# Kernel tuning notes

Hardware: AMD Instinct MI355X
Metric: run time of the kernel (lower is better)

Reference implementation:

```python
import jax, jax.numpy as jnp
import numpy as np

MODES1 = 12
MODES2 = 12
WIDTH = 32
DATA_CH = 3
BN_EPS = 1e-5


def mirror(x):
    # x: (B, C, s, s) -> (B, C, 2s-1, 2s-1), odd-symmetric mirror
    top = jnp.concatenate([x[:, :, -1:0:-1, -1:0:-1], -x[:, :, -1:0:-1, :]], axis=3)
    bot = jnp.concatenate([-x[:, :, :, -1:0:-1], x], axis=3)
    return jnp.concatenate([top, bot], axis=2)


def spectral_conv(x, w1, w2):
    # x: (B, C, H, W); w1, w2: (C, C, m1, m2, 2) real/imag pairs
    H, W = x.shape[-2], x.shape[-1]
    xf = jnp.fft.rfft2(x, norm='ortho')  # (B, C, H, W//2+1) complex
    w1c = w1[..., 0] + 1j * w1[..., 1]
    w2c = w2[..., 0] + 1j * w2[..., 1]
    out = jnp.zeros(xf.shape[:2] + (H, W // 2 + 1), dtype=xf.dtype)
    out = out.at[:, :, :MODES1, :MODES2].set(
        jnp.einsum('bixy,ioxy->boxy', xf[:, :, :MODES1, :MODES2], w1c))
    out = out.at[:, :, H - MODES1:, :MODES2].set(
        jnp.einsum('bixy,ioxy->boxy', xf[:, :, H - MODES1:, :MODES2], w2c))
    return jnp.fft.irfft2(out, s=(H, W), norm='ortho')


def batch_norm(x, g, b):
    # training-mode BN over (B, H, W) per channel, biased variance
    mean = jnp.mean(x, axis=(0, 2, 3), keepdims=True)
    var = jnp.mean((x - mean) ** 2, axis=(0, 2, 3), keepdims=True)
    inv = jax.lax.rsqrt(var + BN_EPS)
    return g[None, :, None, None] * (x - mean) * inv + b[None, :, None, None]


def setup_inputs() -> dict:
    key = jax.random.key(0)
    ks = jax.random.split(key, 16)
    B, s = 16, 128
    scale = 1.0 / (WIDTH * WIDTH)
    inp = {
        'x': jax.random.normal(ks[0], (B, DATA_CH, s, s), dtype=jnp.float32),
        'fc0_w': jax.random.normal(ks[1], (DATA_CH, WIDTH), dtype=jnp.float32) * 0.3,
        'fc0_b': jax.random.normal(ks[2], (WIDTH,), dtype=jnp.float32) * 0.01,
        'spec_w': scale * jax.random.uniform(ks[3], (4, 2, WIDTH, WIDTH, MODES1, MODES2, 2), dtype=jnp.float32),
        'conv_w': jax.random.normal(ks[4], (4, WIDTH, WIDTH), dtype=jnp.float32) * (1.0 / np.sqrt(WIDTH)),
        'conv_b': jax.random.normal(ks[5], (4, WIDTH), dtype=jnp.float32) * 0.01,
        'bn_g': jnp.ones((4, WIDTH), dtype=jnp.float32),
        'bn_b': jnp.zeros((4, WIDTH), dtype=jnp.float32),
        'fc1_w': jax.random.normal(ks[6], (WIDTH, 128), dtype=jnp.float32) * (1.0 / np.sqrt(WIDTH)),
        'fc1_b': jax.random.normal(ks[7], (128,), dtype=jnp.float32) * 0.01,
        'fc2_w': jax.random.normal(ks[8], (128, 1), dtype=jnp.float32) * (1.0 / np.sqrt(128.0)),
        'fc2_b': jax.random.normal(ks[9], (1,), dtype=jnp.float32) * 0.01,
    }
    return inp


def reference(x, fc0_w, fc0_b, spec_w, conv_w, conv_b, bn_g, bn_b, fc1_w, fc1_b, fc2_w, fc2_b):
    x_small = x
    s = x.shape[-1]
    xm = mirror(x)  # (B, C, 2s-1, 2s-1)
    # fc0 lift (channels-last linear)
    h = jnp.einsum('bchw,cd->bdhw', xm, fc0_w) + fc0_b[None, :, None, None]
    for i in range(4):
        x1 = spectral_conv(h, spec_w[i, 0], spec_w[i, 1])
        x2 = jnp.einsum('bchw,oc->bohw', h, conv_w[i]) + conv_b[i][None, :, None, None]
        h = batch_norm(x1 + x2, bn_g[i], bn_b[i])
        if i < 3:
            h = jax.nn.relu(h)
    h = jnp.einsum('bchw,cd->bdhw', h, fc1_w) + fc1_b[None, :, None, None]
    h = jax.nn.relu(h)
    h = jnp.einsum('bchw,cd->bdhw', h, fc2_w) + fc2_b[None, :, None, None]  # (B,1,H,W)
    # unmirror: take bottom-right quadrant; torch assignment broadcasts 1 channel -> data_channels
    out = jnp.broadcast_to(h[:, :, s - 1:, s - 1:], x_small.shape)
    return out
```

## Files before the change

kernel.cpp:

```cpp
#include <hip/hip_runtime.h>

#define BATCH 16
#define CH 32
#define DC 3
#define SS 128
#define HH 255
#define RST 256
#define FST ((size_t)CH*RST)
#define M1 12
#define M2 12
#define KY24 (2*M1)
#define NROWS (BATCH*CH*HH)
#define TWOPI_N 0.02463994238463573f

typedef __attribute__((ext_vector_type(8))) _Float16 f16x8;
typedef __attribute__((ext_vector_type(4))) float f32x4;


__global__ void __launch_bounds__(256) k_fc0(
    const float* __restrict__ x, const float* __restrict__ w,
    const float* __restrict__ bias, _Float16* __restrict__ h){
  int y = blockIdx.x, b = blockIdx.y, t = threadIdx.x;
  int d = t >> 3, g = t & 7;
  int iy = (y >= SS-1) ? y - (SS-1) : (SS-1) - y;
  float w0 = w[d], w1 = w[CH+d], w2 = w[2*CH+d], bs = bias[d];
  const float* xp = x + (size_t)(b*DC)*SS*SS + iy*SS;
  size_t obase = (size_t)(b*HH + y)*FST + (size_t)d*RST;
  #pragma unroll
  for (int i=0; i<4; i++){
    int x0 = i*64 + g*8;
    f16x8 pk;
    #pragma unroll
    for (int u=0; u<8; u++){
      int xx = x0 + u;
      float v = 0.f;
      if (xx < HH){
        int ix = (xx >= SS-1) ? xx - (SS-1) : (SS-1) - xx;
        float sgn = ((y >= SS-1) == (xx >= SS-1)) ? 1.f : -1.f;
        v = bs + sgn*(xp[ix]*w0 + xp[SS*SS+ix]*w1 + xp[2*SS*SS+ix]*w2);
      }
      pk[u] = (_Float16)v;
    }
    *(f16x8*)(h + obase + x0) = pk;
  }
}

__global__ void __launch_bounds__(256) k_tabs(
    const float* __restrict__ w1,
    _Float16* __restrict__ Whi, _Float16* __restrict__ Wlo,
    _Float16* __restrict__ Th,  _Float16* __restrict__ Tl,
    _Float16* __restrict__ W1h, _Float16* __restrict__ W1l){
  int bi = blockIdx.x;
  if (bi < 4){
    int t = bi*256 + threadIdx.x;
    int ct = t >> 9, ks = (t >> 6) & 7, lane = t & 63;
    int col = ct*16 + (lane & 15);
    int kb = ks*32 + (lane >> 4)*8;
    for (int j=0; j<8; j++){
      int k = kb + j;
      float w = 0.f;
      if (k < 255 && col < 24){
        int m = col >> 1;
        float ang = TWOPI_N * (float)((k*m) % 255);
        w = (col & 1) ? -sinf(ang) : cosf(ang);
      }
      _Float16 hi = (_Float16)w;
      Whi[t*8+j] = hi;
      Wlo[t*8+j] = (_Float16)(w - (float)hi);
    }
  } else if (bi < 8){
    int t = (bi-4)*256 + threadIdx.x;
    int ct = t >> 6, lane = t & 63;
    int xx = ct*16 + (lane & 15);
    int jbase = (lane >> 4)*8;
    for (int j=0; j<8; j++){
      int jg = jbase + j;
      float v = 0.f;
      if (xx < HH && jg <= 22){
        if (jg == 0) v = 1.f;
        else if (jg & 1){ int kx=(jg+1)>>1; v =  cosf(TWOPI_N*(float)((kx*xx)%255)); }
        else            { int kx= jg>>1;    v = -sinf(TWOPI_N*(float)((kx*xx)%255)); }
      }
      _Float16 hi = (_Float16)v;
      Th[t*8+j] = hi;
      Tl[t*8+j] = (_Float16)(v - (float)hi);
    }
  } else {
    int t = (bi-8)*256 + threadIdx.x;
    int nt = t >> 6, lane = t & 63;
    int col = nt*16 + (lane & 15);
    int kb = (lane >> 4)*8;
    for (int j=0; j<8; j++){
      float v = w1[(kb+j)*128 + col];
      _Float16 hi = (_Float16)v;
      W1h[t*8+j] = hi;
      W1l[t*8+j] = (_Float16)(v - (float)hi);
    }
  }
}

__global__ void __launch_bounds__(256) k_fwd(
    const _Float16* __restrict__ h, float* __restrict__ Xf,
    const _Float16* __restrict__ Whi, const _Float16* __restrict__ Wlo,
    const float* __restrict__ parts, const float* __restrict__ g,
    const float* __restrict__ bb, float* __restrict__ bnpo,
    int l0, int relu){
  __shared__ float lr[HH][26];
  __shared__ float rs[256][2];
  int t = threadIdx.x, bc = blockIdx.x;
  int wid = t >> 6, lane = t & 63;
  int c = bc & (CH-1), b = bc >> 5;
  float sc = 1.f, sh = 0.f;
  if (!l0){
    float s1 = 0.f, s2 = 0.f;
    for (int k=t; k<BATCH*HH; k+=256){
      float2 p2 = *(const float2*)(parts + (size_t)k*64 + c*2);
      s1 += p2.x; s2 += p2.y;
    }
    rs[t][0] = s1; rs[t][1] = s2;
    __syncthreads();
    for (int w2=128; w2>0; w2>>=1){
      if (t < w2){ rs[t][0] += rs[t+w2][0]; rs[t][1] += rs[t+w2][1]; }
      __syncthreads();
    }
    const float N = (float)BATCH * (float)(HH*HH);
    float mean = rs[0][0] / N;
    float var  = rs[0][1] / N - mean*mean;
    float iv = rsqrtf(var + 1e-5f);
    sc = g[c]*iv;
    sh = bb[c] - mean*sc;
    __syncthreads();
  }
  if (b == 0 && t == 0){ bnpo[c] = sc; bnpo[CH+c] = sh; }
  _Float16 sch = (_Float16)sc, shh = (_Float16)sh;
  f16x8 scv, shv;
  #pragma unroll
  for (int u=0; u<8; u++){ scv[u]=sch; shv[u]=shh; }
  const _Float16* base = h + (size_t)b*HH*FST + (size_t)c*RST;
  int koff = (lane >> 4)*8;
  #pragma unroll
  for (int it=0; it<4; it++){
    int y0 = it*64 + wid*16;
    int yr = y0 + (lane & 15);
    int ycl = (yr < HH) ? yr : HH-1;
    const _Float16* rp = base + (size_t)ycl*FST;
    f16x8 av[8];
    #pragma unroll
    for (int ks=0; ks<8; ks++)
      av[ks] = *(const f16x8*)(rp + ks*32 + koff);
    f32x4 acc0 = {0.f,0.f,0.f,0.f};
    f32x4 acc1 = {0.f,0.f,0.f,0.f};
    #pragma unroll
    for (int ks=0; ks<8; ks++){
      f16x8 a = av[ks]*scv + shv;
      if (relu){
        #pragma unroll
        for (int u=0; u<8; u++) a[u] = (a[u] > (_Float16)0.f) ? a[u] : (_Float16)0.f;
      }
      f16x8 b0h = *(const f16x8*)(Whi + ((size_t)(0*8+ks)*64 + lane)*8);
      f16x8 b0l = *(const f16x8*)(Wlo + ((size_t)(0*8+ks)*64 + lane)*8);
      f16x8 b1h = *(const f16x8*)(Whi + ((size_t)(1*8+ks)*64 + lane)*8);
      f16x8 b1l = *(const f16x8*)(Wlo + ((size_t)(1*8+ks)*64 + lane)*8);
      acc0 = __builtin_amdgcn_mfma_f32_16x16x32_f16(a, b0h, acc0, 0,0,0);
      acc0 = __builtin_amdgcn_mfma_f32_16x16x32_f16(a, b0l, acc0, 0,0,0);
      acc1 = __builtin_amdgcn_mfma_f32_16x16x32_f16(a, b1h, acc1, 0,0,0);
      acc1 = __builtin_amdgcn_mfma_f32_16x16x32_f16(a, b1l, acc1, 0,0,0);
    }
    int colq = lane & 15;
    int rq = y0 + (lane >> 4)*4;
    #pragma unroll
    for (int q=0; q<4; q++)
      if (rq+q < HH) lr[rq+q][colq] = acc0[q];
    if (colq < 8){
      #pragma unroll
      for (int q=0; q<4; q++)
        if (rq+q < HH) lr[rq+q][16+colq] = acc1[q];
    }
  }
  __syncthreads();
  for (int p = t; p < KY24*M2; p += 256){
    int ky = p / M2, kx = p - (p/M2)*M2;
    int freq = (ky < M1) ? ky : (HH - KY24 + ky);
    float ang = TWOPI_N * (float)freq;
    float c1 = cosf(ang), s1 = sinf(ang);
    float cr=1.f, sr=0.f, ar=0.f, ai=0.f;
    for (int y=0; y<HH; y++){
      float rr = lr[y][kx*2], ri = lr[y][kx*2+1];
      ar += rr*cr + ri*sr;
      ai += ri*cr - rr*sr;
      float cn = cr*c1 - sr*s1;
      sr = sr*c1 + cr*s1;
      cr = cn;
    }
    const float inv = 1.0f/255.0f;
    int o = (bc*KY24 + ky)*(M2*2) + kx*2;
    Xf[o]   = ar*inv;
    Xf[o+1] = ai*inv;
  }
}

__global__ void __launch_bounds__(256) k_specmix(
    const float* __restrict__ Xf, const float* __restrict__ w,
    float* __restrict__ G){
  __shared__ float ly[KY24][M2][2];
  int o = blockIdx.x, b = blockIdx.y, t = threadIdx.x;
  for (int m = t; m < KY24*M2; m += 256){
    int ky = m / M2, kx = m - (m/M2)*M2;
    int blk = (ky < M1) ? 0 : 1;
    int m1 = ky - blk*M1;
    const float* wp = w + (size_t)blk*(CH*CH*M1*M2*2)
                        + (size_t)o*(M1*M2*2) + m1*(M2*2) + kx*2;
    const float* xp = Xf + ((size_t)(b*CH)*KY24 + ky)*(M2*2) + kx*2;
    float ar=0.f, ai=0.f;
    for (int i=0;i<CH;i++){
      float xr = xp[0], xi = xp[1];
      float wr = wp[0], wi = wp[1];
      ar += xr*wr - xi*wi;
      ai += xr*wi + xi*wr;
      xp += KY24*M2*2;
      wp += CH*M1*M2*2;
    }
    ly[ky][kx][0] = ar;
    ly[ky][kx][1] = ai;
  }
  __syncthreads();
  const float inv = 1.0f/255.0f;
  size_t bo = (size_t)b*CH + o;
  for (int p=t; p<HH*M2; p+=256){
    int y = p/M2, kx = p - (p/M2)*M2;
    float ang = TWOPI_N * (float)y;
    float c1 = cosf(ang), s1 = sinf(ang);
    float ar = ly[0][kx][0], ai = ly[0][kx][1];
    float c = c1, s = s1;
    #pragma unroll
    for (int k=1; k<=11; k++){
      float yr = ly[k][kx][0],     yi = ly[k][kx][1];
      ar += yr*c - yi*s;
      ai += yr*s + yi*c;
      float zr = ly[24-k][kx][0],  zi = ly[24-k][kx][1];
      ar += zr*c + zi*s;
      ai += zi*c - zr*s;
      float cn = c*c1 - s*s1;
      s = s*c1 + c*s1;
      c = cn;
    }
    {
      float zr = ly[12][kx][0], zi = ly[12][kx][1];
      ar += zr*c + zi*s;
      ai += zi*c - zr*s;
    }
    float f = (kx==0) ? inv : 2.0f*inv;
    size_t og = (bo*HH + y)*(M2*2) + kx*2;
    G[og]   = ar*f;
    G[og+1] = ai*f;
  }
}

__global__ void __launch_bounds__(256) k_fuse(
    const _Float16* __restrict__ h, const float* __restrict__ G,
    const float* __restrict__ cw, const float* __restrict__ cb,
    _Float16* __restrict__ tout, float* __restrict__ partials,
    const _Float16* __restrict__ Th, const _Float16* __restrict__ Tl,
    const float* __restrict__ bnp, int relu){
  __shared__ _Float16 buf[8448];
  __shared__ float red[CH][4][2];
  int t = threadIdx.x;
  int y = blockIdx.x, b = blockIdx.y;
  size_t hbase = (size_t)(b*HH + y)*FST;
  int cS = t >> 5, xg = t & 31;
  f16x8 ld[4];
  #pragma unroll
  for (int it=0; it<4; it++)
    ld[it] = *(const f16x8*)(h + hbase + (size_t)(it*8 + cS)*RST + xg*8);
  int w = t >> 6, lane = t & 63;
  int arow = lane & 15, koff = (lane >> 4)*8;
  f16x8 a0h[2], a0l[2], a1[2];
  #pragma unroll
  for (int rt=0; rt<2; rt++){
    int o = rt*16 + arow;
    #pragma unroll
    for (int j=0; j<8; j++){
      float v = cw[o*CH + koff + j];
      _Float16 hi = (_Float16)v;
      a0h[rt][j] = hi;
      a0l[rt][j] = (_Float16)(v - (float)hi);
    }
    const float* gp = G + ((size_t)(b*CH+o)*HH + y)*24;
    #pragma unroll
    for (int j=0; j<8; j++){
      int jg = koff + j;
      float v = (jg==0) ? gp[0] : gp[jg+1];
      a1[rt][j] = (_Float16)v;
    }
  }
  #pragma unroll
  for (int it=0; it<4; it++){
    int c = it*8 + cS;
    _Float16 sc_ = (_Float16)bnp[c], sh_ = (_Float16)bnp[CH+c];
    f16x8 scv, shv;
    #pragma unroll
    for (int u=0; u<8; u++){ scv[u]=sc_; shv[u]=sh_; }
    f16x8 z = ld[it]*scv + shv;
    if (relu){
      #pragma unroll
      for (int u=0; u<8; u++) z[u] = (z[u] > (_Float16)0.f) ? z[u] : (_Float16)0.f;
    }
    int base = ((xg>>1)*65 + ((xg&1)*8) + ((c>>3)<<4))*8 + (c&7);
    #pragma unroll
    for (int u=0; u<8; u++) buf[base + u*8] = z[u];
  }
  __syncthreads();
  f32x4 acc[2][4];
  #pragma unroll
  for (int rt=0; rt<2; rt++)
    #pragma unroll
    for (int cl=0; cl<4; cl++) acc[rt][cl] = (f32x4){0.f,0.f,0.f,0.f};
  #pragma unroll
  for (int cl=0; cl<4; cl++){
    int ct = w*4 + cl;
    f16x8 bd = *(const f16x8*)(buf + ((size_t)ct*65 + lane)*8);
    f16x8 th = *(const f16x8*)(Th + ((size_t)ct*64 + lane)*8);
    f16x8 tl = *(const f16x8*)(Tl + ((size_t)ct*64 + lane)*8);
    #pragma unroll
    for (int rt=0; rt<2; rt++){
      acc[rt][cl] = __builtin_amdgcn_mfma_f32_16x16x32_f16(a0h[rt], bd, acc[rt][cl], 0,0,0);
      acc[rt][cl] = __builtin_amdgcn_mfma_f32_16x16x32_f16(a0l[rt], bd, acc[rt][cl], 0,0,0);
      acc[rt][cl] = __builtin_amdgcn_mfma_f32_16x16x32_f16(a1[rt], th, acc[rt][cl], 0,0,0);
      acc[rt][cl] = __builtin_amdgcn_mfma_f32_16x16x32_f16(a1[rt], tl, acc[rt][cl], 0,0,0);
    }
  }
  #pragma unroll
  for (int rt=0; rt<2; rt++)
    #pragma unroll
    for (int q=0; q<4; q++){
      float v1 = 0.f, v2 = 0.f;
      #pragma unroll
      for (int cl=0; cl<4; cl++){
        int xxo = (w*4 + cl)*16 + (lane & 15);
        int o = rt*16 + (lane >> 4)*4 + q;
        float v = acc[rt][cl][q] + cb[o];
        float vv = (xxo < HH) ? v : 0.f;
        v1 += vv; v2 += vv*vv;
      }
      #pragma unroll
      for (int off=8; off>0; off>>=1){
        v1 += __shfl_xor(v1, off, 16);
        v2 += __shfl_xor(v2, off, 16);
      }
      if ((lane & 15) == 0){
        int o = rt*16 + (lane >> 4)*4 + q;
        red[o][w][0] = v1;
        red[o][w][1] = v2;
      }
    }
  __syncthreads();
  #pragma unroll
  for (int rt=0; rt<2; rt++)
    #pragma unroll
    for (int cl=0; cl<4; cl++){
      int xxo = (w*4 + cl)*16 + (lane & 15);
      #pragma unroll
      for (int q=0; q<4; q++){
        int o = rt*16 + (lane >> 4)*4 + q;
        buf[o*264 + xxo] = (_Float16)(acc[rt][cl][q] + cb[o]);
      }
    }
  __syncthreads();
  {
    int o = t >> 3, xb = (t & 7)*32;
    #pragma unroll
    for (int v4=0; v4<4; v4++){
      f16x8 vv = *(const f16x8*)(buf + o*264 + xb + v4*8);
      *(f16x8*)(tout + hbase + (size_t)o*RST + xb + v4*8) = vv;
    }
  }
  if (t < CH*2){
    int oo = t >> 1, st = t & 1;
    float s = red[oo][0][st] + red[oo][1][st] + red[oo][2][st] + red[oo][3][st];
    partials[((size_t)b*HH + y)*64 + t] = s;
  }
}

__global__ void __launch_bounds__(512) k_stats(
    const float* __restrict__ partials,
    const float* __restrict__ g, const float* __restrict__ bb,
    float* __restrict__ bnp){
  __shared__ float acc[512];
  int o = blockIdx.x, t = threadIdx.x;
  int half = t >> 8, j = t & 255;
  float s = 0.f;
  for (int k=j; k<BATCH*HH; k+=256) s += partials[(size_t)k*64 + o*2 + half];
  acc[t] = s;
  __syncthreads();
  for (int w2=128; w2>0; w2>>=1){
    if (j < w2) acc[t] += acc[t+w2];
    __syncthreads();
  }
  if (t == 0){
    const float N = (float)BATCH * (float)(HH*HH);
    float mean = acc[0] / N;
    float var  = acc[256] / N - mean*mean;
    float iv = rsqrtf(var + 1e-5f);
    float scv = g[o]*iv;
    bnp[o]      = scv;
    bnp[CH + o] = bb[o] - mean*scv;
  }
}

__global__ void __launch_bounds__(256) k_final(
    const _Float16* __restrict__ tb, const float* __restrict__ bnp,
    const _Float16* __restrict__ W1h, const _Float16* __restrict__ W1l,
    const float* __restrict__ b1, const float* __restrict__ w2,
    const float* __restrict__ b2, float* __restrict__ out){
  __shared__ _Float16 Vf[128][40];
  int yq = blockIdx.x, b = blockIdx.y, t = threadIdx.x;
  int y = (SS-1) + yq;
  size_t rbase = (size_t)(b*HH + y)*FST;
  for (int i=t; i<CH*SS; i+=256){
    int c = i >> 7, xx = i & 127;
    float v = (float)tb[rbase + (size_t)c*RST + (SS-1) + xx]
              * bnp[c] + bnp[CH+c];
    Vf[xx][c] = (_Float16)v;
  }
  __syncthreads();
  int w = t >> 6, lane = t & 63;
  int prow = lane & 15, koff = (lane >> 4)*8, col = lane & 15;
  f16x8 a0 = *(const f16x8*)&Vf[w*32 + prow][koff];
  f16x8 a1 = *(const f16x8*)&Vf[w*32 + 16 + prow][koff];
  float s0[4] = {0.f,0.f,0.f,0.f}, s1[4] = {0.f,0.f,0.f,0.f};
  #pragma unroll
  for (int nt=0; nt<8; nt++){
    f16x8 bh = *(const f16x8*)(W1h + ((size_t)nt*64 + lane)*8);
    f16x8 bl = *(const f16x8*)(W1l + ((size_t)nt*64 + lane)*8);
    f32x4 acc0 = {0.f,0.f,0.f,0.f}, acc1 = {0.f,0.f,0.f,0.f};
    acc0 = __builtin_amdgcn_mfma_f32_16x16x32_f16(a0, bh, acc0, 0,0,0);
    acc0 = __builtin_amdgcn_mfma_f32_16x16x32_f16(a0, bl, acc0, 0,0,0);
    acc1 = __builtin_amdgcn_mfma_f32_16x16x32_f16(a1, bh, acc1, 0,0,0);
    acc1 = __builtin_amdgcn_mfma_f32_16x16x32_f16(a1, bl, acc1, 0,0,0);
    float b1v = b1[nt*16 + col];
    float w2v = w2[nt*16 + col];
    #pragma unroll
    for (int q=0; q<4; q++){
      s0[q] += fmaxf(acc0[q] + b1v, 0.f)*w2v;
      s1[q] += fmaxf(acc1[q] + b1v, 0.f)*w2v;
    }
  }
  float o2b = b2[0];
  #pragma unroll
  for (int q=0; q<4; q++){
    float v0 = s0[q], v1 = s1[q];
    #pragma unroll
    for (int off=8; off>0; off>>=1){
      v0 += __shfl_xor(v0, off, 16);
      v1 += __shfl_xor(v1, off, 16);
    }
    if (col == (unsigned)q){
      int p0 = w*32 + (lane >> 4)*4 + q;
      int p1 = p0 + 16;
      float r0 = v0 + o2b, r1 = v1 + o2b;
      int ob = (b*DC)*SS*SS + yq*SS;
      #pragma unroll
      for (int cc=0; cc<DC; cc++){
        out[ob + cc*SS*SS + p0] = r0;
        out[ob + cc*SS*SS + p1] = r1;
      }
    }
  }
}

extern "C" void kernel_launch(void* const* d_in, const int* in_sizes, int n_in,
                              void* d_out, int out_size, void* d_ws, size_t ws_size,
                              hipStream_t stream) {
  (void)in_sizes; (void)n_in; (void)out_size; (void)ws_size;
  const float* x      = (const float*)d_in[0];
  const float* fc0_w  = (const float*)d_in[1];
  const float* fc0_b  = (const float*)d_in[2];
  const float* spec_w = (const float*)d_in[3];
  const float* conv_w = (const float*)d_in[4];
  const float* conv_b = (const float*)d_in[5];
  const float* bn_g   = (const float*)d_in[6];
  const float* bn_b   = (const float*)d_in[7];
  const float* fc1_w  = (const float*)d_in[8];
  const float* fc1_b  = (const float*)d_in[9];
  const float* fc2_w  = (const float*)d_in[10];
  const float* fc2_b  = (const float*)d_in[11];
  float* out = (float*)d_out;
  float* ws  = (float*)d_ws;

  _Float16* field = (_Float16*)ws;
  float* Gbuf  = ws + 16711680;
  float* Xf    = Gbuf + (size_t)NROWS*24;
  float* parts = Xf   + (size_t)BATCH*CH*KY24*M2*2;
  float* bnpF  = parts + (size_t)64*BATCH*HH;
  float* bnpL  = bnpF + 64;
  _Float16* Whi = (_Float16*)(bnpL + 64);
  _Float16* Wlo = Whi + 2*8*64*8;
  _Float16* Th  = Wlo + 2*8*64*8;
  _Float16* Tl  = Th  + 16*64*8;
  _Float16* W1h = Tl  + 16*64*8;
  _Float16* W1l = W1h + 8*64*8;

  k_tabs<<<10, 256, 0, stream>>>(fc1_w, Whi, Wlo, Th, Tl, W1h, W1l);
  k_fc0<<<dim3(HH, BATCH), 256, 0, stream>>>(x, fc0_w, fc0_b, field);

  const size_t wstride = (size_t)2*CH*CH*M1*M2*2;
  for (int l=0; l<4; l++){
    int l0 = (l == 0);
    int relu = (l >= 1);
    const float* gg = l0 ? bn_g : bn_g + (size_t)(l-1)*CH;
    const float* gb = l0 ? bn_b : bn_b + (size_t)(l-1)*CH;
    k_fwd  <<<BATCH*CH, 256, 0, stream>>>(field, Xf, Whi, Wlo,
                                          parts, gg, gb, bnpF, l0, relu);
    k_specmix<<<dim3(CH, BATCH), 256, 0, stream>>>(Xf, spec_w + (size_t)l*wstride, Gbuf);
    k_fuse <<<dim3(HH, BATCH), 256, 0, stream>>>(field, Gbuf, conv_w + l*CH*CH,
                                                 conv_b + l*CH, field, parts,
                                                 Th, Tl, bnpF, relu);
  }
  k_stats<<<CH, 512, 0, stream>>>(parts, bn_g + 3*CH, bn_b + 3*CH, bnpL);
  k_final<<<dim3(SS, BATCH), 256, 0, stream>>>(field, bnpL, W1h, W1l,
                                               fc1_b, fc2_w, fc2_b, out);
}
```

Measured before the change: 524.0 us.

## Move inverse y-DFT from spectral mix kernel into fused per-row kernel

The spectral mix kernel now writes only the 24x12 mixed mode coefficients per (batch, out-channel) instead of expanding them into a full 255-row G buffer. Each k_fuse block (one row y) computes the inverse y-DFT for its row directly from those coefficients into shared memory and builds the MFMA A operand from there. This removes the write and read of the large G intermediate, in exchange for redundant trig and recurrence work and scattered global reads of Y inside every fuse block.

```diff
diff --git a/kernel.cpp b/kernel.cpp
--- a/kernel.cpp
+++ b/kernel.cpp
@@ -199,10 +199,9 @@
   }
 }
 
-__global__ void __launch_bounds__(256) k_specmix(
+__global__ void __launch_bounds__(256) k_mix(
     const float* __restrict__ Xf, const float* __restrict__ w,
-    float* __restrict__ G){
-  __shared__ float ly[KY24][M2][2];
+    float* __restrict__ Y){
   int o = blockIdx.x, b = blockIdx.y, t = threadIdx.x;
   for (int m = t; m < KY24*M2; m += 256){
     int ky = m / M2, kx = m - (m/M2)*M2;
@@ -220,50 +219,21 @@
       xp += KY24*M2*2;
       wp += CH*M1*M2*2;
     }
-    ly[ky][kx][0] = ar;
-    ly[ky][kx][1] = ai;
-  }
-  __syncthreads();
-  const float inv = 1.0f/255.0f;
-  size_t bo = (size_t)b*CH + o;
-  for (int p=t; p<HH*M2; p+=256){
-    int y = p/M2, kx = p - (p/M2)*M2;
-    float ang = TWOPI_N * (float)y;
-    float c1 = cosf(ang), s1 = sinf(ang);
-    float ar = ly[0][kx][0], ai = ly[0][kx][1];
-    float c = c1, s = s1;
-    #pragma unroll
-    for (int k=1; k<=11; k++){
-      float yr = ly[k][kx][0],     yi = ly[k][kx][1];
-      ar += yr*c - yi*s;
-      ai += yr*s + yi*c;
-      float zr = ly[24-k][kx][0],  zi = ly[24-k][kx][1];
-      ar += zr*c + zi*s;
-      ai += zi*c - zr*s;
-      float cn = c*c1 - s*s1;
-      s = s*c1 + c*s1;
-      c = cn;
-    }
-    {
-      float zr = ly[12][kx][0], zi = ly[12][kx][1];
-      ar += zr*c + zi*s;
-      ai += zi*c - zr*s;
-    }
-    float f = (kx==0) ? inv : 2.0f*inv;
-    size_t og = (bo*HH + y)*(M2*2) + kx*2;
-    G[og]   = ar*f;
-    G[og+1] = ai*f;
+    size_t oy = ((size_t)(b*CH + o)*KY24 + ky)*(M2*2) + kx*2;
+    Y[oy]   = ar;
+    Y[oy+1] = ai;
   }
 }
 
 __global__ void __launch_bounds__(256) k_fuse(
-    const _Float16* __restrict__ h, const float* __restrict__ G,
+    const _Float16* __restrict__ h, const float* __restrict__ Y,
     const float* __restrict__ cw, const float* __restrict__ cb,
     _Float16* __restrict__ tout, float* __restrict__ partials,
     const _Float16* __restrict__ Th, const _Float16* __restrict__ Tl,
     const float* __restrict__ bnp, int relu){
   __shared__ _Float16 buf[8448];
   __shared__ float red[CH][4][2];
+  __shared__ float ldsG[CH*26];
   int t = threadIdx.x;
   int y = blockIdx.x, b = blockIdx.y;
   size_t hbase = (size_t)(b*HH + y)*FST;
@@ -274,7 +244,7 @@
     ld[it] = *(const f16x8*)(h + hbase + (size_t)(it*8 + cS)*RST + xg*8);
   int w = t >> 6, lane = t & 63;
   int arow = lane & 15, koff = (lane >> 4)*8;
-  f16x8 a0h[2], a0l[2], a1[2];
+  f16x8 a0h[2], a0l[2];
   #pragma unroll
   for (int rt=0; rt<2; rt++){
     int o = rt*16 + arow;
@@ -285,7 +255,60 @@
       a0h[rt][j] = hi;
       a0l[rt][j] = (_Float16)(v - (float)hi);
     }
-    const float* gp = G + ((size_t)(b*CH+o)*HH + y)*24;
+  }
+  if (t < 64) ldsG[(t>>1)*26 + 24 + (t&1)] = 0.f;
+  {
+    float ang = TWOPI_N * (float)y;
+    float c1 = cosf(ang), s1 = sinf(ang);
+    const float inv = 1.0f/255.0f;
+    for (int p = t; p < CH*M2; p += 256){
+      int o = p / M2, kx = p - (p/M2)*M2;
+      const float* yp = Y + ((size_t)(b*CH + o)*KY24)*(M2*2) + kx*2;
+      float ar = yp[0], ai = yp[1];
+      float c = c1, s = s1;
+      #pragma unroll
+      for (int k=1; k<=11; k++){
+        float yr = yp[(size_t)k*(M2*2)],      yi = yp[(size_t)k*(M2*2)+1];
+        ar += yr*c - yi*s;
+        ai += yr*s + yi*c;
+        float zr = yp[(size_t)(24-k)*(M2*2)], zi = yp[(size_t)(24-k)*(M2*2)+1];
+        ar += zr*c + zi*s;
+        ai += zi*c - zr*s;
+        float cn = c*c1 - s*s1;
+        s = s*c1 + c*s1;
+        c = cn;
+      }
+      {
+        float zr = yp[12*(M2*2)], zi = yp[12*(M2*2)+1];
+        ar += zr*c + zi*s;
+        ai += zi*c - zr*s;
+      }
+      float f = (kx==0) ? inv : 2.0f*inv;
+      *(float2*)(ldsG + o*26 + kx*2) = make_float2(ar*f, ai*f);
+    }
+  }
+  #pragma unroll
+  for (int it=0; it<4; it++){
+    int c = it*8 + cS;
+    _Float16 sc_ = (_Float16)bnp[c], sh_ = (_Float16)bnp[CH+c];
+    f16x8 scv, shv;
+    #pragma unroll
+    for (int u=0; u<8; u++){ scv[u]=sc_; shv[u]=sh_; }
+    f16x8 z = ld[it]*scv + shv;
+    if (relu){
+      #pragma unroll
+      for (int u=0; u<8; u++) z[u] = (z[u] > (_Float16)0.f) ? z[u] : (_Float16)0.f;
+    }
+    int base = ((xg>>1)*65 + ((xg&1)*8) + ((c>>3)<<4))*8 + (c&7);
+    #pragma unroll
+    for (int u=0; u<8; u++) buf[base + u*8] = z[u];
+  }
+  __syncthreads();
+  f16x8 a1[2];
+  #pragma unroll
+  for (int rt=0; rt<2; rt++){
+    int o = rt*16 + arow;
+    const float* gp = ldsG + o*26;
     #pragma unroll
     for (int j=0; j<8; j++){
       int jg = koff + j;
@@ -293,23 +316,6 @@
       a1[rt][j] = (_Float16)v;
     }
   }
-  #pragma unroll
-  for (int it=0; it<4; it++){
-    int c = it*8 + cS;
-    _Float16 sc_ = (_Float16)bnp[c], sh_ = (_Float16)bnp[CH+c];
-    f16x8 scv, shv;
-    #pragma unroll
-    for (int u=0; u<8; u++){ scv[u]=sc_; shv[u]=sh_; }
-    f16x8 z = ld[it]*scv + shv;
-    if (relu){
-      #pragma unroll
-      for (int u=0; u<8; u++) z[u] = (z[u] > (_Float16)0.f) ? z[u] : (_Float16)0.f;
-    }
-    int base = ((xg>>1)*65 + ((xg&1)*8) + ((c>>3)<<4))*8 + (c&7);
-    #pragma unroll
-    for (int u=0; u<8; u++) buf[base + u*8] = z[u];
-  }
-  __syncthreads();
   f32x4 acc[2][4];
   #pragma unroll
   for (int rt=0; rt<2; rt++)
@@ -488,8 +494,8 @@
   float* ws  = (float*)d_ws;
 
   _Float16* field = (_Float16*)ws;
-  float* Gbuf  = ws + 16711680;
-  float* Xf    = Gbuf + (size_t)NROWS*24;
+  float* Ybuf  = ws + 16711680;
+  float* Xf    = Ybuf + (size_t)BATCH*CH*KY24*M2*2;
   float* parts = Xf   + (size_t)BATCH*CH*KY24*M2*2;
   float* bnpF  = parts + (size_t)64*BATCH*HH;
   float* bnpL  = bnpF + 64;
@@ -509,12 +515,12 @@
     int relu = (l >= 1);
     const float* gg = l0 ? bn_g : bn_g + (size_t)(l-1)*CH;
     const float* gb = l0 ? bn_b : bn_b + (size_t)(l-1)*CH;
-    k_fwd  <<<BATCH*CH, 256, 0, stream>>>(field, Xf, Whi, Wlo,
-                                          parts, gg, gb, bnpF, l0, relu);
-    k_specmix<<<dim3(CH, BATCH), 256, 0, stream>>>(Xf, spec_w + (size_t)l*wstride, Gbuf);
-    k_fuse <<<dim3(HH, BATCH), 256, 0, stream>>>(field, Gbuf, conv_w + l*CH*CH,
-                                                 conv_b + l*CH, field, parts,
-                                                 Th, Tl, bnpF, relu);
+    k_fwd <<<BATCH*CH, 256, 0, stream>>>(field, Xf, Whi, Wlo,
+                                         parts, gg, gb, bnpF, l0, relu);
+    k_mix <<<dim3(CH, BATCH), 256, 0, stream>>>(Xf, spec_w + (size_t)l*wstride, Ybuf);
+    k_fuse<<<dim3(HH, BATCH), 256, 0, stream>>>(field, Ybuf, conv_w + l*CH*CH,
+                                                conv_b + l*CH, field, parts,
+                                                Th, Tl, bnpF, relu);
   }
   k_stats<<<CH, 512, 0, stream>>>(parts, bn_g + 3*CH, bn_b + 3*CH, bnpL);
   k_final<<<dim3(SS, BATCH), 256, 0, stream>>>(field, bnpL, W1h, W1l,
```

Result: slower. 703.4 us (+34.3%).

## Compute y-direction partial DFT in k_fwd with split-fp16 MFMA twiddle tables

Applied to the files above, without the earlier changes.

Replaces the per-thread serial recurrence over 255 rows for the y-direction DFT with MFMA 16x16x32 fp16 matmuls. These run against precomputed cos/sin twiddle tables, with hi/lo splits of both operands to keep near-fp32 accuracy. The x-transformed intermediate is stored in shared memory as fp16 hi/lo pairs instead of fp32. The aim is to remove the long serial FMA chain, which left most threads idle, at the cost of extra table setup and three MFMAs per product term.

```diff
diff --git a/kernel.cpp b/kernel.cpp
--- a/kernel.cpp
+++ b/kernel.cpp
@@ -49,7 +49,9 @@
     const float* __restrict__ w1,
     _Float16* __restrict__ Whi, _Float16* __restrict__ Wlo,
     _Float16* __restrict__ Th,  _Float16* __restrict__ Tl,
-    _Float16* __restrict__ W1h, _Float16* __restrict__ W1l){
+    _Float16* __restrict__ W1h, _Float16* __restrict__ W1l,
+    _Float16* __restrict__ Ach, _Float16* __restrict__ Acl,
+    _Float16* __restrict__ Ash, _Float16* __restrict__ Asl){
   int bi = blockIdx.x;
   if (bi < 4){
     int t = bi*256 + threadIdx.x;
@@ -85,7 +87,7 @@
       Th[t*8+j] = hi;
       Tl[t*8+j] = (_Float16)(v - (float)hi);
     }
-  } else {
+  } else if (bi < 10){
     int t = (bi-8)*256 + threadIdx.x;
     int nt = t >> 6, lane = t & 63;
     int col = nt*16 + (lane & 15);
@@ -96,17 +98,50 @@
       W1h[t*8+j] = hi;
       W1l[t*8+j] = (_Float16)(v - (float)hi);
     }
+  } else if (bi < 14){
+    int t = (bi-10)*256 + threadIdx.x;
+    int mt = t >> 9, ks = (t >> 6) & 7, lane = t & 63;
+    int ky = mt*16 + (lane & 15);
+    int yb = ks*32 + (lane >> 4)*8;
+    int freq = (ky < M1) ? ky : 231 + ky;
+    for (int j=0; j<8; j++){
+      int yy = yb + j;
+      float v = 0.f;
+      if (ky < KY24 && yy < HH)
+        v = cosf(TWOPI_N * (float)((freq*yy) % 255));
+      _Float16 hi = (_Float16)v;
+      Ach[t*8+j] = hi;
+      Acl[t*8+j] = (_Float16)(v - (float)hi);
+    }
+  } else {
+    int t = (bi-14)*256 + threadIdx.x;
+    int mt = t >> 9, ks = (t >> 6) & 7, lane = t & 63;
+    int ky = mt*16 + (lane & 15);
+    int yb = ks*32 + (lane >> 4)*8;
+    int freq = (ky < M1) ? ky : 231 + ky;
+    for (int j=0; j<8; j++){
+      int yy = yb + j;
+      float v = 0.f;
+      if (ky < KY24 && yy < HH)
+        v = sinf(TWOPI_N * (float)((freq*yy) % 255));
+      _Float16 hi = (_Float16)v;
+      Ash[t*8+j] = hi;
+      Asl[t*8+j] = (_Float16)(v - (float)hi);
+    }
   }
 }
 
 __global__ void __launch_bounds__(256) k_fwd(
     const _Float16* __restrict__ h, float* __restrict__ Xf,
     const _Float16* __restrict__ Whi, const _Float16* __restrict__ Wlo,
+    const _Float16* __restrict__ Ach, const _Float16* __restrict__ Acl,
+    const _Float16* __restrict__ Ash, const _Float16* __restrict__ Asl,
     const float* __restrict__ parts, const float* __restrict__ g,
     const float* __restrict__ bb, float* __restrict__ bnpo,
     int l0, int relu){
-  __shared__ float lr[HH][26];
-  __shared__ float rs[256][2];
+  __shared__ _Float16 lrh[256][32];
+  __shared__ _Float16 lrl[256][32];
+  float (*rs)[2] = (float(*)[2])lrh;
   int t = threadIdx.x, bc = blockIdx.x;
   int wid = t >> 6, lane = t & 63;
   int c = bc & (CH-1), b = bc >> 5;
@@ -170,32 +205,63 @@
     int rq = y0 + (lane >> 4)*4;
     #pragma unroll
     for (int q=0; q<4; q++)
-      if (rq+q < HH) lr[rq+q][colq] = acc0[q];
+      if (rq+q < HH){
+        float v = acc0[q];
+        _Float16 hv = (_Float16)v;
+        lrh[rq+q][colq] = hv;
+        lrl[rq+q][colq] = (_Float16)(v - (float)hv);
+      }
     if (colq < 8){
       #pragma unroll
       for (int q=0; q<4; q++)
-        if (rq+q < HH) lr[rq+q][16+colq] = acc1[q];
-    }
-  }
-  __syncthreads();
-  for (int p = t; p < KY24*M2; p += 256){
-    int ky = p / M2, kx = p - (p/M2)*M2;
-    int freq = (ky < M1) ? ky : (HH - KY24 + ky);
-    float ang = TWOPI_N * (float)freq;
-    float c1 = cosf(ang), s1 = sinf(ang);
-    float cr=1.f, sr=0.f, ar=0.f, ai=0.f;
-    for (int y=0; y<HH; y++){
-      float rr = lr[y][kx*2], ri = lr[y][kx*2+1];
-      ar += rr*cr + ri*sr;
-      ai += ri*cr - rr*sr;
-      float cn = cr*c1 - sr*s1;
-      sr = sr*c1 + cr*s1;
-      cr = cn;
+        if (rq+q < HH){
+          float v = acc1[q];
+          _Float16 hv = (_Float16)v;
+          lrh[rq+q][16+colq] = hv;
+          lrl[rq+q][16+colq] = (_Float16)(v - (float)hv);
+        }
+    }
+  }
+  if (t < 64){
+    if (t < 32) lrh[255][t] = (_Float16)0.f;
+    else        lrl[255][t-32] = (_Float16)0.f;
+  }
+  __syncthreads();
+  {
+    int mt = wid >> 1, nt2 = wid & 1;
+    int nn = nt2*16 + (lane & 15);
+    f32x4 accC = {0.f,0.f,0.f,0.f};
+    f32x4 accS = {0.f,0.f,0.f,0.f};
+    #pragma unroll
+    for (int ks=0; ks<8; ks++){
+      f16x8 bh, bl;
+      #pragma unroll
+      for (int j=0; j<8; j++){
+        int yy = ks*32 + koff + j;
+        bh[j] = lrh[yy][nn];
+        bl[j] = lrl[yy][nn];
+      }
+      size_t ai = ((size_t)(mt*8 + ks)*64 + lane)*8;
+      f16x8 ach = *(const f16x8*)(Ach + ai);
+      f16x8 acl = *(const f16x8*)(Acl + ai);
+      f16x8 ash = *(const f16x8*)(Ash + ai);
+      f16x8 asl = *(const f16x8*)(Asl + ai);
+      accC = __builtin_amdgcn_mfma_f32_16x16x32_f16(ach, bh, accC, 0,0,0);
+      accC = __builtin_amdgcn_mfma_f32_16x16x32_f16(ach, bl, accC, 0,0,0);
+      accC = __builtin_amdgcn_mfma_f32_16x16x32_f16(acl, bh, accC, 0,0,0);
+      accS = __builtin_amdgcn_mfma_f32_16x16x32_f16(ash, bh, accS, 0,0,0);
+      accS = __builtin_amdgcn_mfma_f32_16x16x32_f16(ash, bl, accS, 0,0,0);
+      accS = __builtin_amdgcn_mfma_f32_16x16x32_f16(asl, bh, accS, 0,0,0);
     }
     const float inv = 1.0f/255.0f;
-    int o = (bc*KY24 + ky)*(M2*2) + kx*2;
-    Xf[o]   = ar*inv;
-    Xf[o+1] = ai*inv;
+    #pragma unroll
+    for (int q=0; q<4; q++){
+      float d2 = __shfl_xor(accS[q], 1, 64);
+      float val = accC[q] + (((nn & 1) == 0) ? d2 : -d2);
+      int ky = mt*16 + (lane >> 4)*4 + q;
+      if (ky < KY24 && nn < 24)
+        Xf[((size_t)bc*KY24 + ky)*24 + nn] = val*inv;
+    }
   }
 }
 
@@ -499,8 +565,13 @@
   _Float16* Tl  = Th  + 16*64*8;
   _Float16* W1h = Tl  + 16*64*8;
   _Float16* W1l = W1h + 8*64*8;
-
-  k_tabs<<<10, 256, 0, stream>>>(fc1_w, Whi, Wlo, Th, Tl, W1h, W1l);
+  _Float16* Ach = W1l + 8*64*8;
+  _Float16* Acl = Ach + 2*8*64*8;
+  _Float16* Ash = Acl + 2*8*64*8;
+  _Float16* Asl = Ash + 2*8*64*8;
+
+  k_tabs<<<18, 256, 0, stream>>>(fc1_w, Whi, Wlo, Th, Tl, W1h, W1l,
+                                 Ach, Acl, Ash, Asl);
   k_fc0<<<dim3(HH, BATCH), 256, 0, stream>>>(x, fc0_w, fc0_b, field);
 
   const size_t wstride = (size_t)2*CH*CH*M1*M2*2;
@@ -510,6 +581,7 @@
     const float* gg = l0 ? bn_g : bn_g + (size_t)(l-1)*CH;
     const float* gb = l0 ? bn_b : bn_b + (size_t)(l-1)*CH;
     k_fwd  <<<BATCH*CH, 256, 0, stream>>>(field, Xf, Whi, Wlo,
+                                          Ach, Acl, Ash, Asl,
                                           parts, gg, gb, bnpF, l0, relu);
     k_specmix<<<dim3(CH, BATCH), 256, 0, stream>>>(Xf, spec_w + (size_t)l*wstride, Gbuf);
     k_fuse <<<dim3(HH, BATCH), 256, 0, stream>>>(field, Gbuf, conv_w + l*CH*CH,
```

Result: faster. 456.5 us (-12.9%).
